# Kernel optimization log

Measured on AMD Instinct MI355X. Metric: run time of the kernel, lower is better.

The kernel has to match this reference:

```python
import jax, jax.numpy as jnp
import numpy as np

B, T, S, K, H, V = 8, 100, 400, 8, 512, 32000

def setup_inputs() -> dict:
    key = jax.random.key(0)
    ks = jax.random.split(key, 8)
    return {
        "dec_out": jax.random.normal(ks[0], (B, T, H), jnp.float32),
        "W": jax.random.normal(ks[1], (H, V), jnp.float32) * (1.0 / np.sqrt(H)),
        "b": jnp.zeros((V,), jnp.float32),
        "weights": jax.random.uniform(ks[2], (B, T, S), jnp.float32),
        "p_trans": jax.random.uniform(ks[3], (B, T, 1), jnp.float32),
        "trans_probs": jax.random.uniform(ks[4], (B, S, K), jnp.float32),
        "probs": jax.random.uniform(ks[5], (B, S, K), jnp.float32),
        "idxes": jax.random.randint(ks[6], (B, S, K), 0, V, jnp.int64),
    }

def reference(dec_out, W, b, weights, p_trans, trans_probs, probs, idxes):
    # Generator: linear + softmax over vocab -> (B, T, V)
    scores = jax.nn.softmax(jnp.einsum('bth,hv->btv', dec_out, W) + b, axis=-1)
    # Mask translation probs where source prob <= 0.05
    tp = trans_probs * (probs > 0.05).astype(trans_probs.dtype)  # (B, S, K)
    # scatter_add along vocab dim: tmp[b, s, idxes[b, s, k]] += tp[b, s, k]
    bi = jnp.arange(B)[:, None, None]
    si = jnp.arange(S)[None, :, None]
    tmp = jnp.zeros((B, S, V), dec_out.dtype).at[bi, si, idxes].add(tp)
    # blend copy distribution through attention weights
    trans_scores = jnp.einsum('bts,bsv->btv', weights, tmp)
    return jnp.log(p_trans * trans_scores + (1.0 - p_trans) * scores)
```

## Files before the change

kernel.cpp:

```cpp
#include <hip/hip_runtime.h>

#define Bdim 8
#define Tdim 100
#define Sdim 400
#define Kk   8
#define Hdim 512
#define Vdim 32000
#define Mdim 800
#define VCHUNK 4000

typedef __attribute__((ext_vector_type(8))) short short8;
typedef __attribute__((ext_vector_type(4))) short short4v;
typedef __attribute__((ext_vector_type(4))) float float4_t;

static __device__ __forceinline__ unsigned short f2bf(float f) {
    unsigned int x = __float_as_uint(f);
    return (unsigned short)((x + 0x7fffu + ((x >> 16) & 1u)) >> 16);
}
static __device__ __forceinline__ float bf2f(unsigned short h) {
    return __uint_as_float(((unsigned int)h) << 16);
}

static __device__ __forceinline__ void gload_lds16(const void* g, void* s) {
    __builtin_amdgcn_global_load_lds((const __attribute__((address_space(1))) void*)g,
                                     (__attribute__((address_space(3))) void*)s, 16, 0, 0);
}

__global__ void convert_a_kernel(const float* __restrict__ A, unsigned short* __restrict__ Abf,
                                 float* __restrict__ rowsum, int n4) {
    int i = blockIdx.x * blockDim.x + threadIdx.x;
    if (i < Mdim) rowsum[i] = 0.f;
    if (i < n4) {
        float4 f = ((const float4*)A)[i];
        short4v s;
        s[0] = (short)f2bf(f.x); s[1] = (short)f2bf(f.y);
        s[2] = (short)f2bf(f.z); s[3] = (short)f2bf(f.w);
        *(short4v*)(Abf + i * 4) = s;
    }
}

__global__ __launch_bounds__(256) void transpose_kernel(const float* __restrict__ W,
                                                        unsigned short* __restrict__ WT) {
    __shared__ float tile[64][65];
    const int k0 = blockIdx.y * 64;
    const int v0 = blockIdx.x * 64;
    const int t  = threadIdx.x;
    const int tx = t & 15;
    const int ty = t >> 4;
#pragma unroll
    for (int i = 0; i < 64; i += 16) {
        float4 f = *(const float4*)&W[(size_t)(k0 + ty + i) * Vdim + v0 + tx * 4];
        tile[ty + i][tx * 4 + 0] = f.x;
        tile[ty + i][tx * 4 + 1] = f.y;
        tile[ty + i][tx * 4 + 2] = f.z;
        tile[ty + i][tx * 4 + 3] = f.w;
    }
    __syncthreads();
    const int c = t & 7;
    const int v = t >> 3;
#pragma unroll
    for (int i = 0; i < 64; i += 32) {
        short8 s;
#pragma unroll
        for (int j = 0; j < 8; ++j) s[j] = (short)f2bf(tile[c * 8 + j][v + i]);
        *(short8*)&WT[(size_t)(v0 + v + i) * Hdim + k0 + c * 8] = s;
    }
}

__global__ __launch_bounds__(256) void gemm_kernel(const unsigned short* __restrict__ Abf,
                                                   const unsigned short* __restrict__ WT,
                                                   const float* __restrict__ bias,
                                                   unsigned short* __restrict__ logitsbf,
                                                   float* __restrict__ rowsum) {
    __shared__ __align__(16) unsigned short As[2 * 128 * 64];
    __shared__ __align__(16) unsigned short Bs[2 * 128 * 64];

    const int tid  = threadIdx.x;
    const int lane = tid & 63;
    const int wave = tid >> 6;
    const int l15  = lane & 15;
    const int kq   = lane >> 4;

    const int NWG = 7 * 250;
    const int orig = blockIdx.x;
    const int xcd = orig & 7;
    const int q8  = NWG >> 3;
    const int r8  = NWG & 7;
    const int wg  = (xcd < r8 ? xcd * (q8 + 1) : r8 * (q8 + 1) + (xcd - r8) * q8) + (orig >> 3);
    const int m_blk = (wg % 7) * 128;
    const int n_blk = (wg / 7) * 128;

    const int wm = wave & 1, wn = wave >> 1;
    const int m0 = wm * 64, n0 = wn * 64;

    const unsigned short* agp[4];
    const unsigned short* bgp[4];
    int lslot[4];
#pragma unroll
    for (int q = 0; q < 4; ++q) {
        int chunk = (q * 4 + wave) * 64 + lane;
        int row = chunk >> 3, c = chunk & 7;
        int gc  = c ^ (row & 7);
        int arow = m_blk + row;
        if (arow >= Mdim) arow = Mdim - 1;
        agp[q] = Abf + (size_t)arow * Hdim + gc * 8;
        bgp[q] = WT + (size_t)(n_blk + row) * Hdim + gc * 8;
        lslot[q] = (q * 4 + wave) * 512;
    }

    int a_off[2][4], b_off[2][4];
#pragma unroll
    for (int ks = 0; ks < 2; ++ks)
#pragma unroll
        for (int i = 0; i < 4; ++i) {
            int ra = m0 + i * 16 + l15;
            a_off[ks][i] = ra * 64 + (((ks * 4 + kq) ^ (ra & 7)) * 8);
            int rb = n0 + i * 16 + l15;
            b_off[ks][i] = rb * 64 + (((ks * 4 + kq) ^ (rb & 7)) * 8);
        }

    float4_t acc[4][4] = {};

#pragma unroll
    for (int q = 0; q < 4; ++q) {
        gload_lds16(agp[q], As + lslot[q]);
        gload_lds16(bgp[q], Bs + lslot[q]);
    }

    int cur = 0;
#pragma unroll
    for (int kt = 0; kt < 8; ++kt) {
        asm volatile("s_waitcnt vmcnt(0)" ::: "memory");
        __builtin_amdgcn_s_barrier();
        __builtin_amdgcn_sched_barrier(0);
        if (kt < 7) {
            const int ko = (kt + 1) * 64;
            const int nb = (cur ^ 1) * 8192;
#pragma unroll
            for (int q = 0; q < 4; ++q) {
                gload_lds16(agp[q] + ko, As + nb + lslot[q]);
                gload_lds16(bgp[q] + ko, Bs + nb + lslot[q]);
            }
        }
        const unsigned short* Ab = As + cur * 8192;
        const unsigned short* Bb = Bs + cur * 8192;
#pragma unroll
        for (int ks = 0; ks < 2; ++ks) {
            short8 af[4], bfr[4];
#pragma unroll
            for (int i = 0; i < 4; ++i) af[i]  = *(const short8*)(Ab + a_off[ks][i]);
#pragma unroll
            for (int j = 0; j < 4; ++j) bfr[j] = *(const short8*)(Bb + b_off[ks][j]);
#pragma unroll
            for (int i = 0; i < 4; ++i)
#pragma unroll
                for (int j = 0; j < 4; ++j)
                    acc[i][j] = __builtin_amdgcn_mfma_f32_16x16x32_bf16(af[i], bfr[j], acc[i][j], 0, 0, 0);
        }
        cur ^= 1;
    }

    float bj[4];
#pragma unroll
    for (int j = 0; j < 4; ++j) bj[j] = bias[n_blk + n0 + j * 16 + l15];

#pragma unroll
    for (int i = 0; i < 4; ++i) {
        float se[4] = {0.f, 0.f, 0.f, 0.f};
        int grow0 = m_blk + m0 + i * 16 + kq * 4;
#pragma unroll
        for (int j = 0; j < 4; ++j) {
            int col = n_blk + n0 + j * 16 + l15;
#pragma unroll
            for (int r = 0; r < 4; ++r) {
                float v = acc[i][j][r] + bj[j];
                se[r] += __expf(v);
                if (grow0 + r < Mdim)
                    logitsbf[(size_t)(grow0 + r) * Vdim + col] = f2bf(v);
            }
        }
#pragma unroll
        for (int r = 0; r < 4; ++r) {
#pragma unroll
            for (int off = 8; off; off >>= 1)
                se[r] += __shfl_xor(se[r], off, 64);
        }
        if (l15 == 0) {
#pragma unroll
            for (int r = 0; r < 4; ++r)
                if (grow0 + r < Mdim) atomicAdd(&rowsum[grow0 + r], se[r]);
        }
    }
}

__global__ __launch_bounds__(256) void combine_kernel(const unsigned short* __restrict__ logitsbf,
                                                      const float* __restrict__ weights,
                                                      const float* __restrict__ p_trans,
                                                      const float* __restrict__ trans_probs,
                                                      const float* __restrict__ probs,
                                                      const int* __restrict__ idxes,
                                                      const float* __restrict__ rowsum,
                                                      float* __restrict__ out) {
    __shared__ __align__(16) float ts[VCHUNK];

    const int bt  = blockIdx.x;
    const int c   = blockIdx.y;
    const int b   = bt / Tdim;
    const int tid = threadIdx.x;
    const int v0  = c * VCHUNK;

    const float pt = p_trans[bt];
    const float c1 = (1.f - pt) / rowsum[bt];

    float4* ts4 = (float4*)ts;
    const float4 z = make_float4(0.f, 0.f, 0.f, 0.f);
#pragma unroll
    for (int i = tid; i < VCHUNK / 4; i += 256) ts4[i] = z;
    __syncthreads();

    for (int i = tid; i < Sdim * Kk; i += 256) {
        float pv  = probs[b * (Sdim * Kk) + i];
        float tpv = trans_probs[b * (Sdim * Kk) + i];
        int   idx = idxes[b * (Sdim * Kk) + i];
        int   rel = idx - v0;
        if (pv > 0.05f && (unsigned)rel < (unsigned)VCHUNK) {
            float w = weights[bt * Sdim + (i >> 3)];
            atomicAdd(&ts[rel], w * tpv);
        }
    }
    __syncthreads();

    const short8* lrow8 = (const short8*)(logitsbf + (size_t)bt * Vdim + v0);
    float4* out4 = (float4*)(out + (size_t)bt * Vdim + v0);
#pragma unroll
    for (int i = tid; i < VCHUNK / 8; i += 256) {
        short8 x8 = lrow8[i];
        float4 t0 = ts4[i * 2];
        float4 t1 = ts4[i * 2 + 1];
        float4 o0, o1;
        o0.x = __logf(pt * t0.x + c1 * __expf(bf2f((unsigned short)x8[0])));
        o0.y = __logf(pt * t0.y + c1 * __expf(bf2f((unsigned short)x8[1])));
        o0.z = __logf(pt * t0.z + c1 * __expf(bf2f((unsigned short)x8[2])));
        o0.w = __logf(pt * t0.w + c1 * __expf(bf2f((unsigned short)x8[3])));
        o1.x = __logf(pt * t1.x + c1 * __expf(bf2f((unsigned short)x8[4])));
        o1.y = __logf(pt * t1.y + c1 * __expf(bf2f((unsigned short)x8[5])));
        o1.z = __logf(pt * t1.z + c1 * __expf(bf2f((unsigned short)x8[6])));
        o1.w = __logf(pt * t1.w + c1 * __expf(bf2f((unsigned short)x8[7])));
        out4[i * 2]     = o0;
        out4[i * 2 + 1] = o1;
    }
}

extern "C" void kernel_launch(void* const* d_in, const int* in_sizes, int n_in,
                              void* d_out, int out_size, void* d_ws, size_t ws_size,
                              hipStream_t stream) {
    const float* dec_out     = (const float*)d_in[0];
    const float* W           = (const float*)d_in[1];
    const float* bias        = (const float*)d_in[2];
    const float* weights     = (const float*)d_in[3];
    const float* p_trans     = (const float*)d_in[4];
    const float* trans_probs = (const float*)d_in[5];
    const float* probs       = (const float*)d_in[6];
    const int*   idxes       = (const int*)d_in[7];
    float* out = (float*)d_out;

    char* wsb = (char*)d_ws;
    unsigned short* Abf      = (unsigned short*)wsb;
    unsigned short* WT       = (unsigned short*)(wsb + (1ull << 20));
    unsigned short* logitsbf = (unsigned short*)(wsb + (35ull << 20));
    float*          rowsum   = (float*)(wsb + (90ull << 20));

    convert_a_kernel<<<dim3((Mdim * Hdim / 4 + 255) / 256), dim3(256), 0, stream>>>(dec_out, Abf, rowsum, Mdim * Hdim / 4);
    transpose_kernel<<<dim3(Vdim / 64, Hdim / 64), dim3(256), 0, stream>>>(W, WT);
    gemm_kernel<<<dim3(7 * 250), dim3(256), 0, stream>>>(Abf, WT, bias, logitsbf, rowsum);
    combine_kernel<<<dim3(Mdim, Vdim / VCHUNK), dim3(256), 0, stream>>>(logitsbf, weights, p_trans, trans_probs,
                                                                        probs, idxes, rowsum, out);
}
```

Baseline: 286.8 us.

## Restructure GEMM: full-K A tile in LDS, B streamed to registers, 8 waves

The GEMM now loads the whole 128x512 A tile into LDS once per block, swizzled, and streams B fragments directly from global memory into registers with a 4-deep prefetch ring. The double-buffered per-K LDS pipeline is gone. The block grows to 512 threads covering a 128x256 output tile, so the grid is halved. This removes per-K-step barriers and the LDS traffic for B. In exchange it uses 128 KB of LDS per block, issues uncoalesced per-lane global B loads, and depends on the epilogue indexing being correct for the wider N tile.

```diff
diff --git a/kernel.cpp b/kernel.cpp
--- a/kernel.cpp
+++ b/kernel.cpp
@@ -67,13 +67,12 @@
     }
 }
 
-__global__ __launch_bounds__(256) void gemm_kernel(const unsigned short* __restrict__ Abf,
-                                                   const unsigned short* __restrict__ WT,
-                                                   const float* __restrict__ bias,
-                                                   unsigned short* __restrict__ logitsbf,
-                                                   float* __restrict__ rowsum) {
-    __shared__ __align__(16) unsigned short As[2 * 128 * 64];
-    __shared__ __align__(16) unsigned short Bs[2 * 128 * 64];
+__global__ __launch_bounds__(512, 2) void gemm_kernel(const unsigned short* __restrict__ Abf,
+                                                      const unsigned short* __restrict__ WT,
+                                                      const float* __restrict__ bias,
+                                                      unsigned short* __restrict__ logitsbf,
+                                                      float* __restrict__ rowsum) {
+    __shared__ __align__(16) unsigned short As[128 * 512];
 
     const int tid  = threadIdx.x;
     const int lane = tid & 63;
@@ -81,83 +80,70 @@
     const int l15  = lane & 15;
     const int kq   = lane >> 4;
 
-    const int NWG = 7 * 250;
+    const int NWG = 875;
     const int orig = blockIdx.x;
     const int xcd = orig & 7;
     const int q8  = NWG >> 3;
     const int r8  = NWG & 7;
     const int wg  = (xcd < r8 ? xcd * (q8 + 1) : r8 * (q8 + 1) + (xcd - r8) * q8) + (orig >> 3);
     const int m_blk = (wg % 7) * 128;
-    const int n_blk = (wg / 7) * 128;
+    const int n_blk = (wg / 7) * 256;
 
     const int wm = wave & 1, wn = wave >> 1;
     const int m0 = wm * 64, n0 = wn * 64;
 
-    const unsigned short* agp[4];
-    const unsigned short* bgp[4];
-    int lslot[4];
-#pragma unroll
-    for (int q = 0; q < 4; ++q) {
-        int chunk = (q * 4 + wave) * 64 + lane;
-        int row = chunk >> 3, c = chunk & 7;
-        int gc  = c ^ (row & 7);
-        int arow = m_blk + row;
-        if (arow >= Mdim) arow = Mdim - 1;
-        agp[q] = Abf + (size_t)arow * Hdim + gc * 8;
-        bgp[q] = WT + (size_t)(n_blk + row) * Hdim + gc * 8;
-        lslot[q] = (q * 4 + wave) * 512;
-    }
-
-    int a_off[2][4], b_off[2][4];
-#pragma unroll
-    for (int ks = 0; ks < 2; ++ks)
-#pragma unroll
-        for (int i = 0; i < 4; ++i) {
-            int ra = m0 + i * 16 + l15;
-            a_off[ks][i] = ra * 64 + (((ks * 4 + kq) ^ (ra & 7)) * 8);
-            int rb = n0 + i * 16 + l15;
-            b_off[ks][i] = rb * 64 + (((ks * 4 + kq) ^ (rb & 7)) * 8);
-        }
+    const unsigned short* bptr[4];
+#pragma unroll
+    for (int j = 0; j < 4; ++j)
+        bptr[j] = WT + (size_t)(n_blk + n0 + j * 16 + l15) * Hdim + kq * 8;
+
+    short8 bp[4][4];
+#pragma unroll
+    for (int t = 0; t < 4; ++t)
+#pragma unroll
+        for (int j = 0; j < 4; ++j)
+            bp[t][j] = *(const short8*)(bptr[j] + t * 32);
+
+#pragma unroll
+    for (int q = 0; q < 16; ++q) {
+        int slot = q * 512 + tid;
+        int row  = slot >> 6;
+        int c    = slot & 63;
+        int gc   = (c & ~7) | ((c ^ row) & 7);
+        int arow = m_blk + row; if (arow >= Mdim) arow = Mdim - 1;
+        gload_lds16(Abf + (size_t)arow * Hdim + gc * 8,
+                    As + (size_t)(q * 512 + wave * 64) * 8);
+    }
+
+    int abase[4][2];
+#pragma unroll
+    for (int i = 0; i < 4; ++i) {
+        int row = m0 + i * 16 + l15;
+#pragma unroll
+        for (int p = 0; p < 2; ++p)
+            abase[i][p] = row * 512 + (((p * 4 + kq) ^ (row & 7)) * 8);
+    }
 
     float4_t acc[4][4] = {};
 
-#pragma unroll
-    for (int q = 0; q < 4; ++q) {
-        gload_lds16(agp[q], As + lslot[q]);
-        gload_lds16(bgp[q], Bs + lslot[q]);
-    }
-
-    int cur = 0;
-#pragma unroll
-    for (int kt = 0; kt < 8; ++kt) {
-        asm volatile("s_waitcnt vmcnt(0)" ::: "memory");
-        __builtin_amdgcn_s_barrier();
-        __builtin_amdgcn_sched_barrier(0);
-        if (kt < 7) {
-            const int ko = (kt + 1) * 64;
-            const int nb = (cur ^ 1) * 8192;
-#pragma unroll
-            for (int q = 0; q < 4; ++q) {
-                gload_lds16(agp[q] + ko, As + nb + lslot[q]);
-                gload_lds16(bgp[q] + ko, Bs + nb + lslot[q]);
-            }
-        }
-        const unsigned short* Ab = As + cur * 8192;
-        const unsigned short* Bb = Bs + cur * 8192;
-#pragma unroll
-        for (int ks = 0; ks < 2; ++ks) {
-            short8 af[4], bfr[4];
-#pragma unroll
-            for (int i = 0; i < 4; ++i) af[i]  = *(const short8*)(Ab + a_off[ks][i]);
-#pragma unroll
-            for (int j = 0; j < 4; ++j) bfr[j] = *(const short8*)(Bb + b_off[ks][j]);
-#pragma unroll
-            for (int i = 0; i < 4; ++i)
-#pragma unroll
-                for (int j = 0; j < 4; ++j)
-                    acc[i][j] = __builtin_amdgcn_mfma_f32_16x16x32_bf16(af[i], bfr[j], acc[i][j], 0, 0, 0);
-        }
-        cur ^= 1;
+    __syncthreads();
+
+#pragma unroll
+    for (int t = 0; t < 16; ++t) {
+        short8 af[4];
+#pragma unroll
+        for (int i = 0; i < 4; ++i)
+            af[i] = *(const short8*)(As + abase[i][t & 1] + (t >> 1) * 64);
+#pragma unroll
+        for (int i = 0; i < 4; ++i)
+#pragma unroll
+            for (int j = 0; j < 4; ++j)
+                acc[i][j] = __builtin_amdgcn_mfma_f32_16x16x32_bf16(af[i], bp[t & 3][j], acc[i][j], 0, 0, 0);
+        if (t + 4 < 16) {
+#pragma unroll
+            for (int j = 0; j < 4; ++j)
+                bp[t & 3][j] = *(const short8*)(bptr[j] + (t + 4) * 32);
+        }
     }
 
     float bj[4];
@@ -272,7 +258,7 @@
 
     convert_a_kernel<<<dim3((Mdim * Hdim / 4 + 255) / 256), dim3(256), 0, stream>>>(dec_out, Abf, rowsum, Mdim * Hdim / 4);
     transpose_kernel<<<dim3(Vdim / 64, Hdim / 64), dim3(256), 0, stream>>>(W, WT);
-    gemm_kernel<<<dim3(7 * 250), dim3(256), 0, stream>>>(Abf, WT, bias, logitsbf, rowsum);
+    gemm_kernel<<<dim3(875), dim3(512), 0, stream>>>(Abf, WT, bias, logitsbf, rowsum);
     combine_kernel<<<dim3(Mdim, Vdim / VCHUNK), dim3(256), 0, stream>>>(logitsbf, weights, p_trans, trans_probs,
                                                                         probs, idxes, rowsum, out);
 }
```

Result: slower. 318.6 us (+11.1%).
